# Performance work log

Measured on AMD Instinct MI355X. Metric: run time of the kernel, lower is better.

## Reference

```python
import jax, jax.numpy as jnp
import numpy as np

BIT_SIZE = 8
ES_SIZE = 1
IN_F = 2048
OUT_F = 2048
N = 8192


def posit_quantize(x, nbits, es):
    """Round-to-nearest posit(nbits, es) quantization, returned as float32.

    Posit value: sign * useed^k * 2^e * (1+f), useed = 2^(2^es).
    Regime length rlen = k+2 (k>=0) or -k+1 (k<0); fraction bits =
    nbits - 1(sign) - rlen - es, clamped at 0. Magnitudes are clamped to
    [minpos, maxpos] (posits never round a nonzero value to zero/inf).
    """
    two_es = 2 ** es                      # useed = 2**two_es
    npat = nbits - 2
    maxpos = jnp.float32(2.0 ** (two_es * npat))
    minpos = jnp.float32(2.0 ** (-two_es * npat))

    sign = jnp.sign(x)
    ax = jnp.clip(jnp.abs(x), minpos, maxpos)

    s = jnp.floor(jnp.log2(ax))           # integer power-of-two scale
    k = jnp.floor(s / two_es)             # regime value
    rlen = jnp.where(k >= 0, k + 2.0, -k + 1.0)
    fbits = jnp.maximum(nbits - 1.0 - rlen - es, 0.0)

    m = ax * jnp.exp2(-s)                 # mantissa in [1, 2)
    fscale = jnp.exp2(fbits)
    mq = jnp.round(m * fscale) / fscale   # round fraction to fbits
    # carry: mantissa rounded up to 2.0 -> bump exponent
    s = jnp.where(mq >= 2.0, s + 1.0, s)
    mq = jnp.where(mq >= 2.0, 1.0, mq)

    y = sign * mq * jnp.exp2(s)
    y = jnp.clip(y, -maxpos, maxpos)
    return jnp.where(x == 0, jnp.float32(0.0), y).astype(x.dtype)


def setup_inputs() -> dict:
    key = jax.random.key(0)
    kx, kw, kb = jax.random.split(key, 3)
    x = jax.random.normal(kx, (N, IN_F), dtype=jnp.float32)
    bound = 1.0 / np.sqrt(IN_F)  # nn.Linear default init range
    weight = jax.random.uniform(kw, (OUT_F, IN_F), dtype=jnp.float32,
                                minval=-bound, maxval=bound)
    bias = jax.random.uniform(kb, (OUT_F,), dtype=jnp.float32,
                              minval=-bound, maxval=bound)
    return {"x": x, "weight": weight, "bias": bias}


def reference(x, weight, bias):
    xq = posit_quantize(x, BIT_SIZE, ES_SIZE)
    wq = posit_quantize(weight, BIT_SIZE, ES_SIZE)
    bq = posit_quantize(bias, BIT_SIZE, ES_SIZE)
    # y = xq @ wq^T + bq  (nn.Linear)
    return jnp.einsum('ni,oi->no', xq, wq) + bq
```

## Files before the change

kernel.cpp:

```cpp
#include <hip/hip_runtime.h>

typedef __attribute__((ext_vector_type(8))) short bf16x8;
typedef __attribute__((ext_vector_type(4))) float f32x4;

__device__ __forceinline__ float posit_q(float x) {
  float ax = fabsf(x);
  ax = fmaxf(ax, 0x1p-12f);
  ax = fminf(ax, 0x1p12f);
  int s = (int)(__float_as_uint(ax) >> 23) - 127;
  int k = s >> 1;
  int rlen = (k >= 0) ? (k + 2) : (1 - k);
  int fbits = 6 - rlen;
  fbits = fbits < 0 ? 0 : fbits;
  float m = ax * __uint_as_float((unsigned)(127 - s) << 23);
  float fs = (float)(1 << fbits);
  float inv_fs = __uint_as_float((unsigned)(127 - fbits) << 23);
  float mq = rintf(m * fs) * inv_fs;
  if (mq >= 2.0f) { s += 1; mq = 1.0f; }
  float y = mq * __uint_as_float((unsigned)(127 + s) << 23);
  y = fminf(y, 0x1p12f);
  y = copysignf(y, x);
  return (x == 0.0f) ? 0.0f : y;
}

__device__ __forceinline__ ushort4 quant4_bf16(float4 v) {
  ushort4 o;
  o.x = (ushort)(__float_as_uint(posit_q(v.x)) >> 16);
  o.y = (ushort)(__float_as_uint(posit_q(v.y)) >> 16);
  o.z = (ushort)(__float_as_uint(posit_q(v.z)) >> 16);
  o.w = (ushort)(__float_as_uint(posit_q(v.w)) >> 16);
  return o;
}

__global__ void posit_quant_all(const float* __restrict__ x,
                                const float* __restrict__ w,
                                const float* __restrict__ b,
                                ushort* __restrict__ Xq,
                                ushort* __restrict__ Wq,
                                float* __restrict__ bq,
                                int nx4, int nw4, int nb4) {
  int i = blockIdx.x * blockDim.x + threadIdx.x;
  if (i < nx4) {
    ((ushort4*)Xq)[i] = quant4_bf16(((const float4*)x)[i]);
  } else if (i < nx4 + nw4) {
    int j = i - nx4;
    ((ushort4*)Wq)[j] = quant4_bf16(((const float4*)w)[j]);
  } else if (i < nx4 + nw4 + nb4) {
    int j = i - nx4 - nw4;
    float4 v = ((const float4*)b)[j];
    float4 o;
    o.x = posit_q(v.x); o.y = posit_q(v.y);
    o.z = posit_q(v.z); o.w = posit_q(v.w);
    ((float4*)bq)[j] = o;
  }
}

__device__ __forceinline__ void gl_lds16(const ushort* g, ushort* l) {
  __builtin_amdgcn_global_load_lds(
      (const __attribute__((address_space(1))) void*)g,
      (__attribute__((address_space(3))) void*)l,
      16, 0, 0);
}

__global__ __launch_bounds__(512, 4) void posit_gemm(
    const ushort* __restrict__ A, const ushort* __restrict__ B,
    const float* __restrict__ bq, float* __restrict__ C,
    int M, int N, int K) {
  __shared__ ushort sA[256 * 64];
  __shared__ ushort sB[128 * 64];

  const int tid = threadIdx.x;
  const int wave = tid >> 6;
  const int lane = tid & 63;
  const int wm = wave >> 1;
  const int wn = wave & 1;
  const int m0 = blockIdx.y << 8;
  const int n0 = blockIdx.x << 7;

  const int g8 = lane >> 3;
  const int qe = ((lane & 7) ^ g8) << 3;
  const int rb = (wave << 3) + g8;

  const ushort* Ag = A + (size_t)(m0 + rb) * K + qe;
  const ushort* Bg = B + (size_t)(n0 + rb) * K + qe;
  const size_t rstep = (size_t)64 * K;

  const int wbase = wave << 9;
  ushort* lA0 = sA + wbase;
  ushort* lB0 = sB + wbase;

  const int fr = lane & 15;
  const int t4 = lane >> 4;
  const int pk0 = ((t4 ^ (fr & 7)) << 3);
  const int pk1 = (((4 + t4) ^ (fr & 7)) << 3);

  f32x4 acc[4][4];
#pragma unroll
  for (int i = 0; i < 4; i++)
#pragma unroll
    for (int j = 0; j < 4; j++) acc[i][j] = (f32x4){0.f, 0.f, 0.f, 0.f};

  for (int k0 = 0; k0 < K; k0 += 64) {
#pragma unroll
    for (int r = 0; r < 4; r++)
      gl_lds16(Ag + k0 + r * rstep, lA0 + (r << 12));
#pragma unroll
    for (int r = 0; r < 2; r++)
      gl_lds16(Bg + k0 + r * rstep, lB0 + (r << 12));
    __syncthreads();

#pragma unroll
    for (int kk = 0; kk < 2; kk++) {
      const int pk = kk ? pk1 : pk0;
      bf16x8 fa[4], fb[4];
#pragma unroll
      for (int i = 0; i < 4; i++)
        fa[i] = *(const bf16x8*)(sA + (((wm << 6) + (i << 4) + fr) << 6) + pk);
#pragma unroll
      for (int j = 0; j < 4; j++)
        fb[j] = *(const bf16x8*)(sB + (((wn << 6) + (j << 4) + fr) << 6) + pk);

#pragma unroll
      for (int i = 0; i < 4; i++)
#pragma unroll
        for (int j = 0; j < 4; j++)
          acc[i][j] = __builtin_amdgcn_mfma_f32_16x16x32_bf16(
              fa[i], fb[j], acc[i][j], 0, 0, 0);
    }
    __syncthreads();
  }

  const int row0 = m0 + (wm << 6) + (t4 << 2);
  const int col0 = n0 + (wn << 6) + fr;
#pragma unroll
  for (int j = 0; j < 4; j++) {
    const int col = col0 + (j << 4);
    const float bv = bq[col];
#pragma unroll
    for (int i = 0; i < 4; i++) {
      const int row = row0 + (i << 4);
#pragma unroll
      for (int r = 0; r < 4; r++)
        C[(size_t)(row + r) * N + col] = acc[i][j][r] + bv;
    }
  }
}

extern "C" void kernel_launch(void* const* d_in, const int* in_sizes, int n_in,
                              void* d_out, int out_size, void* d_ws, size_t ws_size,
                              hipStream_t stream) {
  const float* x = (const float*)d_in[0];
  const float* w = (const float*)d_in[1];
  const float* bias = (const float*)d_in[2];
  float* out = (float*)d_out;

  const int out_f = in_sizes[2];
  const int in_f = in_sizes[1] / out_f;
  const int m = in_sizes[0] / in_f;
  const int k = in_f;

  ushort* Xq = (ushort*)d_ws;
  ushort* Wq = Xq + (size_t)m * k;
  float* bquant = (float*)(Wq + (size_t)out_f * k);

  const int nx4 = in_sizes[0] / 4;
  const int nw4 = in_sizes[1] / 4;
  const int nb4 = in_sizes[2] / 4;
  const int total4 = nx4 + nw4 + nb4;
  posit_quant_all<<<(total4 + 255) / 256, 256, 0, stream>>>(
      x, w, bias, Xq, Wq, bquant, nx4, nw4, nb4);

  dim3 grid(out_f / 128, m / 256);
  posit_gemm<<<grid, 512, 0, stream>>>(Xq, Wq, bquant, out, m, out_f, k);
}
```

Before: 184.5 us.

## Use 256x256 GEMM tiles with double-buffered LDS and interleaved prefetch

The GEMM block tile grows from 256x128 to 256x256, with each wave computing a 128x64 sub-tile. LDS becomes a two-stage double buffer filled by direct global-to-LDS loads issued two K-steps ahead. Each K-step is split into four MFMA phases separated by barriers and s_setprio, with the next tile's loads interleaved between them. The aim is to hide global-load latency and raise arithmetic intensity per LDS byte. In exchange, register and LDS use go up, occupancy drops to 2 blocks, and the grid has half as many blocks.

```diff
diff --git a/kernel.cpp b/kernel.cpp
--- a/kernel.cpp
+++ b/kernel.cpp
@@ -62,82 +62,163 @@
       16, 0, 0);
 }
 
-__global__ __launch_bounds__(512, 4) void posit_gemm(
+__global__ __launch_bounds__(512, 2) void posit_gemm(
     const ushort* __restrict__ A, const ushort* __restrict__ B,
     const float* __restrict__ bq, float* __restrict__ C,
     int M, int N, int K) {
-  __shared__ ushort sA[256 * 64];
-  __shared__ ushort sB[128 * 64];
+  __shared__ ushort lds[65536];
 
   const int tid = threadIdx.x;
   const int wave = tid >> 6;
   const int lane = tid & 63;
-  const int wm = wave >> 1;
-  const int wn = wave & 1;
+  const int wm = wave >> 2;
+  const int wn = wave & 3;
   const int m0 = blockIdx.y << 8;
-  const int n0 = blockIdx.x << 7;
-
-  const int g8 = lane >> 3;
-  const int qe = ((lane & 7) ^ g8) << 3;
-  const int rb = (wave << 3) + g8;
-
-  const ushort* Ag = A + (size_t)(m0 + rb) * K + qe;
-  const ushort* Bg = B + (size_t)(n0 + rb) * K + qe;
+  const int n0 = blockIdx.x << 8;
+
+  const int srow = tid >> 3;
+  const int scol = ((tid & 7) ^ (srow & 7)) << 3;
+  const ushort* Ag = A + (size_t)(m0 + srow) * K + scol;
+  const ushort* Bg = B + (size_t)(n0 + srow) * K + scol;
   const size_t rstep = (size_t)64 * K;
-
-  const int wbase = wave << 9;
-  ushort* lA0 = sA + wbase;
-  ushort* lB0 = sB + wbase;
+  const int ldst = wave << 9;
+
+  ushort* const sA0 = lds;
+  ushort* const sB0 = lds + 32768;
 
   const int fr = lane & 15;
   const int t4 = lane >> 4;
-  const int pk0 = ((t4 ^ (fr & 7)) << 3);
-  const int pk1 = (((4 + t4) ^ (fr & 7)) << 3);
-
-  f32x4 acc[4][4];
-#pragma unroll
-  for (int i = 0; i < 4; i++)
+  const int swz = fr & 7;
+
+  f32x4 acc[8][4];
+#pragma unroll
+  for (int i = 0; i < 8; i++)
 #pragma unroll
     for (int j = 0; j < 4; j++) acc[i][j] = (f32x4){0.f, 0.f, 0.f, 0.f};
 
-  for (int k0 = 0; k0 < K; k0 += 64) {
-#pragma unroll
-    for (int r = 0; r < 4; r++)
-      gl_lds16(Ag + k0 + r * rstep, lA0 + (r << 12));
-#pragma unroll
-    for (int r = 0; r < 2; r++)
-      gl_lds16(Bg + k0 + r * rstep, lB0 + (r << 12));
-    __syncthreads();
-
-#pragma unroll
-    for (int kk = 0; kk < 2; kk++) {
-      const int pk = kk ? pk1 : pk0;
-      bf16x8 fa[4], fb[4];
-#pragma unroll
-      for (int i = 0; i < 4; i++)
-        fa[i] = *(const bf16x8*)(sA + (((wm << 6) + (i << 4) + fr) << 6) + pk);
-#pragma unroll
-      for (int j = 0; j < 4; j++)
-        fb[j] = *(const bf16x8*)(sB + (((wn << 6) + (j << 4) + fr) << 6) + pk);
-
-#pragma unroll
-      for (int i = 0; i < 4; i++)
-#pragma unroll
-        for (int j = 0; j < 4; j++)
+#pragma unroll
+  for (int r = 0; r < 4; r++) gl_lds16(Ag + r * rstep,      sA0 + (r << 12) + ldst);
+#pragma unroll
+  for (int r = 0; r < 4; r++) gl_lds16(Bg + r * rstep,      sB0 + (r << 12) + ldst);
+#pragma unroll
+  for (int r = 0; r < 4; r++) gl_lds16(Ag + 64 + r * rstep, sA0 + 16384 + (r << 12) + ldst);
+#pragma unroll
+  for (int r = 0; r < 4; r++) gl_lds16(Bg + 64 + r * rstep, sB0 + 16384 + (r << 12) + ldst);
+  asm volatile("s_waitcnt vmcnt(8)" ::: "memory");
+  __builtin_amdgcn_s_barrier();
+
+  const int T = K >> 6;
+  for (int t = 0; t < T; ++t) {
+    ushort* const sAb = sA0 + ((t & 1) << 14);
+    ushort* const sBb = sB0 + ((t & 1) << 14);
+    const bool st = (t + 2) < T;
+    const size_t kt2 = (size_t)(t + 2) << 6;
+
+    bf16x8 fa[4][2], fb[4][2];
+
+#pragma unroll
+    for (int i = 0; i < 4; i++)
+#pragma unroll
+      for (int kk = 0; kk < 2; kk++)
+        fa[i][kk] = *(const bf16x8*)(sAb + ((((wm << 7) + (i << 4) + fr) << 6) +
+                                            (((kk * 4 + t4) ^ swz) << 3)));
+#pragma unroll
+    for (int j = 0; j < 2; j++)
+#pragma unroll
+      for (int kk = 0; kk < 2; kk++)
+        fb[j][kk] = *(const bf16x8*)(sBb + ((((wn << 6) + (j << 4) + fr) << 6) +
+                                            (((kk * 4 + t4) ^ swz) << 3)));
+    __builtin_amdgcn_s_barrier();
+    __builtin_amdgcn_s_setprio(1);
+#pragma unroll
+    for (int kk = 0; kk < 2; kk++)
+#pragma unroll
+      for (int i = 0; i < 4; i++)
+#pragma unroll
+        for (int j = 0; j < 2; j++)
           acc[i][j] = __builtin_amdgcn_mfma_f32_16x16x32_bf16(
-              fa[i], fb[j], acc[i][j], 0, 0, 0);
-    }
-    __syncthreads();
+              fa[i][kk], fb[j][kk], acc[i][j], 0, 0, 0);
+    __builtin_amdgcn_s_setprio(0);
+    __builtin_amdgcn_s_barrier();
+
+#pragma unroll
+    for (int j = 2; j < 4; j++)
+#pragma unroll
+      for (int kk = 0; kk < 2; kk++)
+        fb[j][kk] = *(const bf16x8*)(sBb + ((((wn << 6) + (j << 4) + fr) << 6) +
+                                            (((kk * 4 + t4) ^ swz) << 3)));
+    if (st) {
+      gl_lds16(Ag + kt2 + 0 * rstep, sAb + (0 << 12) + ldst);
+      gl_lds16(Ag + kt2 + 2 * rstep, sAb + (2 << 12) + ldst);
+    }
+    __builtin_amdgcn_s_barrier();
+    __builtin_amdgcn_s_setprio(1);
+#pragma unroll
+    for (int kk = 0; kk < 2; kk++)
+#pragma unroll
+      for (int i = 0; i < 4; i++)
+#pragma unroll
+        for (int j = 2; j < 4; j++)
+          acc[i][j] = __builtin_amdgcn_mfma_f32_16x16x32_bf16(
+              fa[i][kk], fb[j][kk], acc[i][j], 0, 0, 0);
+    __builtin_amdgcn_s_setprio(0);
+    __builtin_amdgcn_s_barrier();
+
+#pragma unroll
+    for (int i = 0; i < 4; i++)
+#pragma unroll
+      for (int kk = 0; kk < 2; kk++)
+        fa[i][kk] = *(const bf16x8*)(sAb + ((((wm << 7) + 64 + (i << 4) + fr) << 6) +
+                                            (((kk * 4 + t4) ^ swz) << 3)));
+    if (st) {
+#pragma unroll
+      for (int r = 0; r < 4; r++)
+        gl_lds16(Bg + kt2 + r * rstep, sBb + (r << 12) + ldst);
+    }
+    __builtin_amdgcn_s_barrier();
+    __builtin_amdgcn_s_setprio(1);
+#pragma unroll
+    for (int kk = 0; kk < 2; kk++)
+#pragma unroll
+      for (int i = 0; i < 4; i++)
+#pragma unroll
+        for (int j = 0; j < 2; j++)
+          acc[i + 4][j] = __builtin_amdgcn_mfma_f32_16x16x32_bf16(
+              fa[i][kk], fb[j][kk], acc[i + 4][j], 0, 0, 0);
+    __builtin_amdgcn_s_setprio(0);
+    __builtin_amdgcn_s_barrier();
+
+    if (st) {
+      gl_lds16(Ag + kt2 + 1 * rstep, sAb + (1 << 12) + ldst);
+      gl_lds16(Ag + kt2 + 3 * rstep, sAb + (3 << 12) + ldst);
+    }
+    __builtin_amdgcn_s_barrier();
+    __builtin_amdgcn_s_setprio(1);
+#pragma unroll
+    for (int kk = 0; kk < 2; kk++)
+#pragma unroll
+      for (int i = 0; i < 4; i++)
+#pragma unroll
+        for (int j = 2; j < 4; j++)
+          acc[i + 4][j] = __builtin_amdgcn_mfma_f32_16x16x32_bf16(
+              fa[i][kk], fb[j][kk], acc[i + 4][j], 0, 0, 0);
+    __builtin_amdgcn_s_setprio(0);
+    if (st) {
+      asm volatile("s_waitcnt vmcnt(8)" ::: "memory");
+    } else if (t + 1 < T) {
+      asm volatile("s_waitcnt vmcnt(0)" ::: "memory");
+    }
+    __builtin_amdgcn_s_barrier();
   }
 
-  const int row0 = m0 + (wm << 6) + (t4 << 2);
+  const int row0 = m0 + (wm << 7) + (t4 << 2);
   const int col0 = n0 + (wn << 6) + fr;
 #pragma unroll
   for (int j = 0; j < 4; j++) {
     const int col = col0 + (j << 4);
     const float bv = bq[col];
 #pragma unroll
-    for (int i = 0; i < 4; i++) {
+    for (int i = 0; i < 8; i++) {
       const int row = row0 + (i << 4);
 #pragma unroll
       for (int r = 0; r < 4; r++)
@@ -170,6 +251,6 @@
   posit_quant_all<<<(total4 + 255) / 256, 256, 0, stream>>>(
       x, w, bias, Xq, Wq, bquant, nx4, nw4, nb4);
 
-  dim3 grid(out_f / 128, m / 256);
+  dim3 grid(out_f / 256, m / 256);
   posit_gemm<<<grid, 512, 0, stream>>>(Xq, Wq, bquant, out, m, out_f, k);
 }
```

After: 193.7 us. +5.0%, slower.

## Rewrite GEMM as 256x256 tile with double-buffered LDS and interleaved loads

Applied to the files above, without the earlier changes.

The GEMM block tile grows from 256x128 to 256x256, with 8 waves laid out 2x4 and each wave owning a 128x64 sub-tile. LDS is double-buffered (128 KB) so global-to-LDS loads for the next K tiles are issued between quarter-step MFMA groups, guarded by explicit vmcnt waits and barriers. s_setprio is raised around the MFMA groups. The aim is to hide global load latency and raise arithmetic intensity per LDS byte. The cost is lower occupancy (launch bounds 2, large LDS use), many barriers, and a grid that is half as large, which may underfill the CUs.

```diff
diff --git a/kernel.cpp b/kernel.cpp
--- a/kernel.cpp
+++ b/kernel.cpp
@@ -62,82 +62,163 @@
       16, 0, 0);
 }
 
-__global__ __launch_bounds__(512, 4) void posit_gemm(
+#define BAR() __builtin_amdgcn_s_barrier()
+#define LGKM0() asm volatile("s_waitcnt lgkmcnt(0)" ::: "memory")
+
+__global__ __launch_bounds__(512, 2) void posit_gemm(
     const ushort* __restrict__ A, const ushort* __restrict__ B,
     const float* __restrict__ bq, float* __restrict__ C,
     int M, int N, int K) {
-  __shared__ ushort sA[256 * 64];
-  __shared__ ushort sB[128 * 64];
+  __shared__ ushort lds[65536];
 
   const int tid = threadIdx.x;
   const int wave = tid >> 6;
   const int lane = tid & 63;
-  const int wm = wave >> 1;
-  const int wn = wave & 1;
+  const int wm = wave >> 2;
+  const int wn = wave & 3;
   const int m0 = blockIdx.y << 8;
-  const int n0 = blockIdx.x << 7;
-
-  const int g8 = lane >> 3;
-  const int qe = ((lane & 7) ^ g8) << 3;
-  const int rb = (wave << 3) + g8;
-
-  const ushort* Ag = A + (size_t)(m0 + rb) * K + qe;
-  const ushort* Bg = B + (size_t)(n0 + rb) * K + qe;
-  const size_t rstep = (size_t)64 * K;
-
-  const int wbase = wave << 9;
-  ushort* lA0 = sA + wbase;
-  ushort* lB0 = sB + wbase;
+  const int n0 = blockIdx.x << 8;
+
+  ushort* const A0 = lds;
+  ushort* const A1 = lds + 16384;
+  ushort* const B0 = lds + 32768;
+  ushort* const B1 = lds + 49152;
+
+  const int l8 = lane >> 3;
+  const int scol = ((lane & 7) ^ l8) << 3;
+  const ushort* Ag = A + (size_t)(m0 + l8) * K + scol;
+  const ushort* Bg = B + (size_t)(n0 + l8) * K + scol;
+
+  const int e0 = wave << 1, e1 = e0 + 1;
+  const int rAlo0 = (e0 << 3) + ((e0 >> 3) << 6);
+  const int rAlo1 = (e1 << 3) + ((e1 >> 3) << 6);
+  const int rAhi0 = rAlo0 + 64, rAhi1 = rAlo1 + 64;
+  const int rBlo0 = ((e0 >> 2) << 6) + ((e0 & 3) << 3);
+  const int rBlo1 = ((e1 >> 2) << 6) + ((e1 & 3) << 3);
+  const int rBhi0 = rBlo0 + 32, rBhi1 = rBlo1 + 32;
+
+#define ST_A(buf, r0, r1, kt) {                                   \
+    gl_lds16(Ag + (size_t)(r0) * K + (kt), (buf) + ((r0) << 6));  \
+    gl_lds16(Ag + (size_t)(r1) * K + (kt), (buf) + ((r1) << 6)); }
+#define ST_B(buf, r0, r1, kt) {                                   \
+    gl_lds16(Bg + (size_t)(r0) * K + (kt), (buf) + ((r0) << 6));  \
+    gl_lds16(Bg + (size_t)(r1) * K + (kt), (buf) + ((r1) << 6)); }
 
   const int fr = lane & 15;
   const int t4 = lane >> 4;
-  const int pk0 = ((t4 ^ (fr & 7)) << 3);
-  const int pk1 = (((4 + t4) ^ (fr & 7)) << 3);
-
-  f32x4 acc[4][4];
-#pragma unroll
-  for (int i = 0; i < 4; i++)
+  const int swz = fr & 7;
+  const int c0 = (t4 ^ swz) << 3;
+  const int c1 = ((4 + t4) ^ swz) << 3;
+  const int arl = ((wm << 7) + fr) << 6;
+  const int brl = ((wn << 6) + fr) << 6;
+
+#define RD_A(dst, base, hi)                                            \
+  _Pragma("unroll") for (int i = 0; i < 4; i++) {                      \
+    dst[i][0] = *(const bf16x8*)((base) + arl + (hi) + (i << 10) + c0);\
+    dst[i][1] = *(const bf16x8*)((base) + arl + (hi) + (i << 10) + c1); }
+#define RD_B(dst, base, jo)                                            \
+  _Pragma("unroll") for (int j = 0; j < 2; j++) {                      \
+    dst[j][0] = *(const bf16x8*)((base) + brl + (((jo) + j) << 10) + c0);\
+    dst[j][1] = *(const bf16x8*)((base) + brl + (((jo) + j) << 10) + c1); }
+
+#define MFMA_Q(AF, BF, I0, J0)                                         \
+  __builtin_amdgcn_s_setprio(1);                                       \
+  _Pragma("unroll") for (int kk = 0; kk < 2; kk++)                     \
+    _Pragma("unroll") for (int i = 0; i < 4; i++)                      \
+      _Pragma("unroll") for (int j = 0; j < 2; j++)                    \
+        acc[(I0) + i][(J0) + j] = __builtin_amdgcn_mfma_f32_16x16x32_bf16( \
+            AF[i][kk], BF[j][kk], acc[(I0) + i][(J0) + j], 0, 0, 0);   \
+  __builtin_amdgcn_s_setprio(0);
+
+  f32x4 acc[8][4];
+#pragma unroll
+  for (int i = 0; i < 8; i++)
 #pragma unroll
     for (int j = 0; j < 4; j++) acc[i][j] = (f32x4){0.f, 0.f, 0.f, 0.f};
 
-  for (int k0 = 0; k0 < K; k0 += 64) {
-#pragma unroll
-    for (int r = 0; r < 4; r++)
-      gl_lds16(Ag + k0 + r * rstep, lA0 + (r << 12));
-#pragma unroll
-    for (int r = 0; r < 2; r++)
-      gl_lds16(Bg + k0 + r * rstep, lB0 + (r << 12));
-    __syncthreads();
-
-#pragma unroll
-    for (int kk = 0; kk < 2; kk++) {
-      const int pk = kk ? pk1 : pk0;
-      bf16x8 fa[4], fb[4];
-#pragma unroll
-      for (int i = 0; i < 4; i++)
-        fa[i] = *(const bf16x8*)(sA + (((wm << 6) + (i << 4) + fr) << 6) + pk);
-#pragma unroll
-      for (int j = 0; j < 4; j++)
-        fb[j] = *(const bf16x8*)(sB + (((wn << 6) + (j << 4) + fr) << 6) + pk);
-
-#pragma unroll
-      for (int i = 0; i < 4; i++)
-#pragma unroll
-        for (int j = 0; j < 4; j++)
-          acc[i][j] = __builtin_amdgcn_mfma_f32_16x16x32_bf16(
-              fa[i], fb[j], acc[i][j], 0, 0, 0);
+  ST_A(A0, rAlo0, rAlo1, 0);
+  ST_B(B0, rBlo0, rBlo1, 0);
+  ST_A(A0, rAhi0, rAhi1, 0);
+  ST_B(B0, rBhi0, rBhi1, 0);
+  ST_B(B1, rBlo0, rBlo1, 64);
+  ST_A(A1, rAhi0, rAhi1, 64);
+  asm volatile("s_waitcnt vmcnt(4)" ::: "memory");
+  BAR();
+
+  const int T = K >> 6;
+  const int U = T >> 1;
+
+#pragma unroll 1
+  for (int u = 0; u < U; ++u) {
+    const int ktb = (u << 7) + 64;
+    const int kt2 = (u << 7) + 128;
+    const int kt3 = (u << 7) + 192;
+    const bool stg = (u + 1 < U);
+
+    bf16x8 falo[4][2], fahi[4][2], fbl[2][2], fbh[2][2];
+
+    RD_A(falo, A0, 0);
+    RD_B(fbl, B0, 0);
+    ST_A(A1, rAlo0, rAlo1, ktb);
+    ST_B(B1, rBhi0, rBhi1, ktb);
+    BAR(); LGKM0();
+    MFMA_Q(falo, fbl, 0, 0);
+    BAR();
+
+    RD_A(fahi, A0, 4096);
+    BAR(); LGKM0();
+    MFMA_Q(fahi, fbl, 4, 0);
+    BAR();
+
+    RD_B(fbh, B0, 2);
+    if (stg) ST_B(B0, rBlo0, rBlo1, kt2);
+    BAR(); LGKM0();
+    MFMA_Q(fahi, fbh, 4, 2);
+    BAR();
+
+    if (stg) ST_A(A0, rAhi0, rAhi1, kt2);
+    BAR();
+    MFMA_Q(falo, fbh, 0, 2);
+    if (stg) { asm volatile("s_waitcnt vmcnt(4)" ::: "memory"); }
+    else     { asm volatile("s_waitcnt vmcnt(0)" ::: "memory"); }
+    BAR();
+
+    RD_A(falo, A1, 0);
+    RD_B(fbl, B1, 0);
+    if (stg) {
+      ST_A(A0, rAlo0, rAlo1, kt2);
+      ST_B(B0, rBhi0, rBhi1, kt2);
     }
-    __syncthreads();
+    BAR(); LGKM0();
+    MFMA_Q(falo, fbl, 0, 0);
+    BAR();
+
+    RD_A(fahi, A1, 4096);
+    BAR(); LGKM0();
+    MFMA_Q(fahi, fbl, 4, 0);
+    BAR();
+
+    RD_B(fbh, B1, 2);
+    if (stg) ST_B(B1, rBlo0, rBlo1, kt3);
+    BAR(); LGKM0();
+    MFMA_Q(fahi, fbh, 4, 2);
+    BAR();
+
+    if (stg) ST_A(A1, rAhi0, rAhi1, kt3);
+    BAR();
+    MFMA_Q(falo, fbh, 0, 2);
+    if (stg) { asm volatile("s_waitcnt vmcnt(4)" ::: "memory"); }
+    BAR();
   }
 
-  const int row0 = m0 + (wm << 6) + (t4 << 2);
+  const int row0 = m0 + (wm << 7) + (t4 << 2);
   const int col0 = n0 + (wn << 6) + fr;
 #pragma unroll
   for (int j = 0; j < 4; j++) {
     const int col = col0 + (j << 4);
     const float bv = bq[col];
 #pragma unroll
-    for (int i = 0; i < 4; i++) {
+    for (int i = 0; i < 8; i++) {
       const int row = row0 + (i << 4);
 #pragma unroll
       for (int r = 0; r < 4; r++)
@@ -170,6 +251,6 @@
   posit_quant_all<<<(total4 + 255) / 256, 256, 0, stream>>>(
       x, w, bias, Xq, Wq, bquant, nx4, nw4, nb4);
 
-  dim3 grid(out_f / 128, m / 256);
+  dim3 grid(out_f / 256, m / 256);
   posit_gemm<<<grid, 512, 0, stream>>>(Xq, Wq, bquant, out, m, out_f, k);
 }
```

New measurement: 208.4 us. +13.0%, slower.

## Double-buffer A tile in LDS and prefetch next k-step during compute

Applied to the files above, without the earlier changes.

Splits the A tile in LDS into two buffers and issues the next k-step's A loads before waiting on the current tile, using partial vmcnt waits and raw barriers in place of __syncthreads. The aim is to overlap global-to-LDS traffic for A with the MFMA work and shorten per-iteration stalls. LDS use grows from 48KB to 80KB per block, which may lower occupancy below the launch-bounds target. The B tile is still loaded synchronously each step.

```diff
diff --git a/kernel.cpp b/kernel.cpp
--- a/kernel.cpp
+++ b/kernel.cpp
@@ -66,8 +66,7 @@
     const ushort* __restrict__ A, const ushort* __restrict__ B,
     const float* __restrict__ bq, float* __restrict__ C,
     int M, int N, int K) {
-  __shared__ ushort sA[256 * 64];
-  __shared__ ushort sB[128 * 64];
+  __shared__ ushort lds[40960];
 
   const int tid = threadIdx.x;
   const int wave = tid >> 6;
@@ -76,6 +75,9 @@
   const int wn = wave & 1;
   const int m0 = blockIdx.y << 8;
   const int n0 = blockIdx.x << 7;
+
+  ushort* const sA = lds;
+  ushort* const sB = lds + 32768;
 
   const int g8 = lane >> 3;
   const int qe = ((lane & 7) ^ g8) << 3;
@@ -86,8 +88,6 @@
   const size_t rstep = (size_t)64 * K;
 
   const int wbase = wave << 9;
-  ushort* lA0 = sA + wbase;
-  ushort* lB0 = sB + wbase;
 
   const int fr = lane & 15;
   const int t4 = lane >> 4;
@@ -100,14 +100,30 @@
 #pragma unroll
     for (int j = 0; j < 4; j++) acc[i][j] = (f32x4){0.f, 0.f, 0.f, 0.f};
 
-  for (int k0 = 0; k0 < K; k0 += 64) {
 #pragma unroll
-    for (int r = 0; r < 4; r++)
-      gl_lds16(Ag + k0 + r * rstep, lA0 + (r << 12));
+  for (int r = 0; r < 4; r++)
+    gl_lds16(Ag + r * rstep, sA + (r << 12) + wbase);
+
+  const int T = K >> 6;
+#pragma unroll 2
+  for (int t = 0; t < T; ++t) {
+    const int k0 = t << 6;
+    ushort* const cur = sA + ((t & 1) << 14);
+
 #pragma unroll
     for (int r = 0; r < 2; r++)
-      gl_lds16(Bg + k0 + r * rstep, lB0 + (r << 12));
-    __syncthreads();
+      gl_lds16(Bg + k0 + r * rstep, sB + (r << 12) + wbase);
+    if (t + 1 < T) {
+      ushort* const nxt = sA + (((t + 1) & 1) << 14);
+#pragma unroll
+      for (int r = 0; r < 4; r++)
+        gl_lds16(Ag + k0 + 64 + r * rstep, nxt + (r << 12) + wbase);
+      asm volatile("s_waitcnt vmcnt(4)" ::: "memory");
+    } else {
+      asm volatile("s_waitcnt vmcnt(0)" ::: "memory");
+    }
+    __builtin_amdgcn_s_barrier();
+    __builtin_amdgcn_sched_barrier(0);
 
 #pragma unroll
     for (int kk = 0; kk < 2; kk++) {
@@ -115,7 +131,7 @@
       bf16x8 fa[4], fb[4];
 #pragma unroll
       for (int i = 0; i < 4; i++)
-        fa[i] = *(const bf16x8*)(sA + (((wm << 6) + (i << 4) + fr) << 6) + pk);
+        fa[i] = *(const bf16x8*)(cur + (((wm << 6) + (i << 4) + fr) << 6) + pk);
 #pragma unroll
       for (int j = 0; j < 4; j++)
         fb[j] = *(const bf16x8*)(sB + (((wn << 6) + (j << 4) + fr) << 6) + pk);
@@ -127,7 +143,7 @@
           acc[i][j] = __builtin_amdgcn_mfma_f32_16x16x32_bf16(
               fa[i], fb[j], acc[i][j], 0, 0, 0);
     }
-    __syncthreads();
+    __builtin_amdgcn_s_barrier();
   }
 
   const int row0 = m0 + (wm << 6) + (t4 << 2);
```

After: 189.8 us. +2.9%, slower.
